# Performance work log

Measured on AMD Instinct MI355X. Metric: run time of the kernel, lower is better.

## Reference

```python
import jax, jax.numpy as jnp
import numpy as np

D_MODEL = 1024
NUM_HEADS = 16
KEY_SIZE = D_MODEL // NUM_HEADS
NEG_BIG = -1.0e9


def setup_inputs() -> dict:
    key = jax.random.key(0)
    ks = jax.random.split(key, 11)
    B, S = 2, 2048
    scale = 1.0 / np.sqrt(D_MODEL)
    inp = {
        "q": jax.random.normal(ks[0], (B, S, D_MODEL), dtype=jnp.float32),
        "v": jax.random.normal(ks[1], (B, S, D_MODEL), dtype=jnp.float32),
        "mask": jnp.ones((B, 1, S, S), dtype=jnp.float32),
        "wq_w": jax.random.normal(ks[2], (D_MODEL, D_MODEL), dtype=jnp.float32) * scale,
        "wq_b": jnp.zeros((D_MODEL,), dtype=jnp.float32),
        "wk_w": jax.random.normal(ks[3], (D_MODEL, D_MODEL), dtype=jnp.float32) * scale,
        "wk_b": jnp.zeros((D_MODEL,), dtype=jnp.float32),
        "wv_w": jax.random.normal(ks[4], (D_MODEL, D_MODEL), dtype=jnp.float32) * scale,
        "wv_b": jnp.zeros((D_MODEL,), dtype=jnp.float32),
        "wo_w": jax.random.normal(ks[5], (D_MODEL, D_MODEL), dtype=jnp.float32) * scale,
        "wo_b": jnp.zeros((D_MODEL,), dtype=jnp.float32),
    }
    return inp


def _split_heads(x, B):
    # [B, S, D] -> [B, H, S, K]
    S = x.shape[1]
    return x.reshape(B, S, NUM_HEADS, KEY_SIZE).transpose(0, 2, 1, 3)


def reference(q, v, mask, wq_w, wq_b, wk_w, wk_b, wv_w, wv_b, wo_w, wo_b):
    B = q.shape[0]
    query = _split_heads(q @ wq_w + wq_b, B)   # [B,H,Sq,K]
    key = _split_heads(v @ wk_w + wk_b, B)     # [B,H,Skv,K]
    value = _split_heads(v @ wv_w + wv_b, B)   # [B,H,Skv,K]

    score = jnp.einsum("bhqd,bhkd->bhqk", query, key) / jnp.sqrt(
        jnp.asarray(KEY_SIZE, dtype=jnp.float32)
    )
    # Original masking: multiply by mask, then replace exact zeros with -1e9.
    score = score * mask
    score = jnp.where(score == 0.0, jnp.float32(NEG_BIG), score)

    alignment = jax.nn.softmax(score, axis=-1)           # [B,H,Sq,Skv]
    context = jnp.einsum("bhqk,bhkd->bhqd", alignment, value)  # [B,H,Sq,K]
    context = context.transpose(0, 2, 1, 3).reshape(B, -1, D_MODEL)
    heads = context @ wo_w + wo_b
    return heads, alignment
```

## Files before the change

kernel.cpp:

```cpp
#include <hip/hip_runtime.h>
#include <cstddef>

#define D 1024
#define H 16
#define S 2048
#define B 2
#define M_ROWS (B * S)
#define NT 16
#define NEG_BIG_F (-1.0e9f)

typedef short bfrag __attribute__((ext_vector_type(8)));
typedef float f32x4 __attribute__((ext_vector_type(4)));

__device__ __forceinline__ unsigned short bf_rn(float x) {
    unsigned u = __float_as_uint(x);
    u += 0x7FFFu + ((u >> 16) & 1u);
    return (unsigned short)(u >> 16);
}
__device__ __forceinline__ float bf2f(unsigned short h) {
    return __uint_as_float(((unsigned)h) << 16);
}

__device__ __forceinline__ void load16(const float4* __restrict__ g, float (&x)[16]) {
#pragma unroll
    for (int q = 0; q < 4; q++) {
        float4 t = g[q];
        x[q*4+0] = t.x; x[q*4+1] = t.y; x[q*4+2] = t.z; x[q*4+3] = t.w;
    }
}

__device__ __forceinline__ void split16_store(const float (&x)[16],
                                              short* __restrict__ hp,
                                              short* __restrict__ lp) {
    __align__(16) short hs[16], ls[16];
#pragma unroll
    for (int e = 0; e < 16; e++) {
        unsigned short hh = bf_rn(x[e]);
        hs[e] = (short)hh;
        ls[e] = (short)bf_rn(x[e] - bf2f(hh));
    }
    *(bfrag*)(hp)     = *(const bfrag*)&hs[0];
    *(bfrag*)(hp + 8) = *(const bfrag*)&hs[8];
    *(bfrag*)(lp)     = *(const bfrag*)&ls[0];
    *(bfrag*)(lp + 8) = *(const bfrag*)&ls[8];
}

#define MFMA3(accv, AH, AL, BH, BL)                                          \
    accv = __builtin_amdgcn_mfma_f32_16x16x32_bf16(AH, BH, accv, 0, 0, 0);   \
    accv = __builtin_amdgcn_mfma_f32_16x16x32_bf16(AH, BL, accv, 0, 0, 0);   \
    accv = __builtin_amdgcn_mfma_f32_16x16x32_bf16(AL, BH, accv, 0, 0, 0);

__global__ __launch_bounds__(256) void transpose_w(
    const float* __restrict__ Win, float* __restrict__ WT)
{
    __shared__ float t[64][65];
    const int tid = threadIdx.x;
    const int bx = blockIdx.x * 64, by = blockIdx.y * 64;
    const int c = tid & 63, r0 = tid >> 6;
#pragma unroll
    for (int r = r0; r < 64; r += 4)
        t[r][c] = Win[(size_t)(by + r) * D + bx + c];
    __syncthreads();
#pragma unroll
    for (int r = r0; r < 64; r += 4)
        WT[(size_t)(bx + r) * D + by + c] = t[c][r];
}

#define PADK 72

__global__ __launch_bounds__(256) void mm_proj(
    const float* __restrict__ A, const float* __restrict__ WT,
    const float* __restrict__ bias, float* __restrict__ Cout, int mode)
{
    __shared__ __align__(16) short Ah[128][PADK], Al[128][PADK];
    __shared__ __align__(16) short Bh[64][PADK],  Bl[64][PADK];

    const int tid  = threadIdx.x;
    const int lane = tid & 63, wid = tid >> 6;
    const int wm = (wid >> 1) * 64, wn = (wid & 1) * 32;
    const int lr = lane >> 4, lc = lane & 15;
    const int tile_n = blockIdx.x * 64;
    const int tile_m = blockIdx.y * 128;

    f32x4 acc[4][2] = {};

    for (int k0 = 0; k0 < D; k0 += 64) {
        __syncthreads();
#pragma unroll
        for (int p = 0; p < 2; p++) {
            int s = tid + p * 256;
            int row = s >> 2, kseg = (s & 3) * 16;
            float x[16];
            load16((const float4*)&A[(size_t)(tile_m + row) * D + k0 + kseg], x);
            split16_store(x, &Ah[row][kseg], &Al[row][kseg]);
        }
        {
            int row = tid >> 2, kseg = (tid & 3) * 16;
            float x[16];
            load16((const float4*)&WT[(size_t)(tile_n + row) * D + k0 + kseg], x);
            split16_store(x, &Bh[row][kseg], &Bl[row][kseg]);
        }
        __syncthreads();
#pragma unroll
        for (int ks = 0; ks < 2; ks++) {
            const int ko = ks * 32 + lr * 8;
            bfrag ah[4], al[4], bh[2], bl[2];
#pragma unroll
            for (int fm = 0; fm < 4; fm++) {
                ah[fm] = *(const bfrag*)&Ah[wm + fm * 16 + lc][ko];
                al[fm] = *(const bfrag*)&Al[wm + fm * 16 + lc][ko];
            }
#pragma unroll
            for (int fn = 0; fn < 2; fn++) {
                bh[fn] = *(const bfrag*)&Bh[wn + fn * 16 + lc][ko];
                bl[fn] = *(const bfrag*)&Bl[wn + fn * 16 + lc][ko];
            }
#pragma unroll
            for (int fm = 0; fm < 4; fm++)
#pragma unroll
                for (int fn = 0; fn < 2; fn++) {
                    MFMA3(acc[fm][fn], ah[fm], al[fm], bh[fn], bl[fn])
                }
        }
    }

#pragma unroll
    for (int fm = 0; fm < 4; fm++)
#pragma unroll
        for (int fn = 0; fn < 2; fn++) {
            const int gm0 = tile_m + wm + fm * 16 + lr * 4;
            const int gn  = tile_n + wn + fn * 16 + lc;
            const float bv = bias[gn];
            if (mode == 2) {
                int bb = gm0 >> 11, ss = gm0 & (S - 1);
                int hh = gn >> 6,  dd = gn & 63;
                float4 o = {acc[fm][fn][0] + bv, acc[fm][fn][1] + bv,
                            acc[fm][fn][2] + bv, acc[fm][fn][3] + bv};
                *(float4*)&Cout[((size_t)(bb * H + hh) * 64 + dd) * S + ss] = o;
            } else {
#pragma unroll
                for (int r = 0; r < 4; r++) {
                    int gm = gm0 + r;
                    float val = acc[fm][fn][r] + bv;
                    if (mode == 0) {
                        Cout[(size_t)gm * D + gn] = val;
                    } else {
                        int bb = gm >> 11, ss = gm & (S - 1);
                        int hh = gn >> 6,  dd = gn & 63;
                        Cout[(((size_t)(bb * H + hh) * S + ss) << 6) + dd] = val;
                    }
                }
            }
        }
}

#define PADK32 40

__global__ __launch_bounds__(256) void scores_mm(
    const float* __restrict__ Q, const float* __restrict__ Kp,
    const float* __restrict__ mask, float* __restrict__ Sc,
    float2* __restrict__ aux)
{
    __shared__ __align__(16) short Qh[128][PADK32], Ql[128][PADK32];
    __shared__ __align__(16) short Kh[128][PADK32], Kl[128][PADK32];
    __shared__ float smx[2][128], sls[2][128];

    const int tid  = threadIdx.x;
    const int lane = tid & 63, wid = tid >> 6;
    const int wm = (wid >> 1) * 64, wn = (wid & 1) * 64;
    const int lr = lane >> 4, lc = lane & 15;
    const int bh = blockIdx.z, b = bh >> 4;
    const int tile_m = blockIdx.y * 128, tile_n = blockIdx.x * 128;

    const float* Qg = Q  + (((size_t)bh * S) << 6);
    const float* Kg = Kp + (((size_t)bh * S) << 6);

    f32x4 acc[4][4] = {};

    for (int k0 = 0; k0 < 64; k0 += 32) {
        __syncthreads();
        const int row = tid >> 1, kseg = (tid & 1) * 16;
        {
            float x[16];
            load16((const float4*)&Qg[((size_t)(tile_m + row) << 6) + k0 + kseg], x);
            split16_store(x, &Qh[row][kseg], &Ql[row][kseg]);
        }
        {
            float x[16];
            load16((const float4*)&Kg[((size_t)(tile_n + row) << 6) + k0 + kseg], x);
            split16_store(x, &Kh[row][kseg], &Kl[row][kseg]);
        }
        __syncthreads();
        const int ko = lr * 8;
        bfrag qh[4], ql[4], kh[4], kl[4];
#pragma unroll
        for (int fm = 0; fm < 4; fm++) {
            qh[fm] = *(const bfrag*)&Qh[wm + fm * 16 + lc][ko];
            ql[fm] = *(const bfrag*)&Ql[wm + fm * 16 + lc][ko];
        }
#pragma unroll
        for (int fn = 0; fn < 4; fn++) {
            kh[fn] = *(const bfrag*)&Kh[wn + fn * 16 + lc][ko];
            kl[fn] = *(const bfrag*)&Kl[wn + fn * 16 + lc][ko];
        }
#pragma unroll
        for (int fm = 0; fm < 4; fm++)
#pragma unroll
            for (int fn = 0; fn < 4; fn++) {
                MFMA3(acc[fm][fn], qh[fm], ql[fm], kh[fn], kl[fn])
            }
    }

    const float* mb = mask + (size_t)b * S * S;
    float* Sh = Sc + (size_t)bh * S * S;
#pragma unroll
    for (int fm = 0; fm < 4; fm++)
#pragma unroll
        for (int r = 0; r < 4; r++) {
            const int lrow = wm + fm * 16 + lr * 4 + r;
            const int gm = tile_m + lrow;
            float sc[4];
#pragma unroll
            for (int fn = 0; fn < 4; fn++) {
                const int gn = tile_n + wn + fn * 16 + lc;
                float v = acc[fm][fn][r] * 0.125f;
                v *= mb[(size_t)gm * S + gn];
                if (v == 0.0f) v = NEG_BIG_F;
                sc[fn] = v;
                Sh[(size_t)gm * S + gn] = v;
            }
            float mx = fmaxf(fmaxf(sc[0], sc[1]), fmaxf(sc[2], sc[3]));
#pragma unroll
            for (int d2 = 1; d2 < 16; d2 <<= 1) mx = fmaxf(mx, __shfl_xor(mx, d2));
            float ls = __expf(sc[0] - mx) + __expf(sc[1] - mx) +
                       __expf(sc[2] - mx) + __expf(sc[3] - mx);
#pragma unroll
            for (int d2 = 1; d2 < 16; d2 <<= 1) ls += __shfl_xor(ls, d2);
            if (lc == 0) { smx[wn >> 6][lrow] = mx; sls[wn >> 6][lrow] = ls; }
        }
    __syncthreads();
    if (tid < 128) {
        float m0 = smx[0][tid], m1 = smx[1][tid];
        float mx = fmaxf(m0, m1);
        float ls = sls[0][tid] * __expf(m0 - mx) + sls[1][tid] * __expf(m1 - mx);
        aux[((size_t)bh * S + tile_m + tid) * NT + blockIdx.x] = make_float2(mx, ls);
    }
}

__global__ __launch_bounds__(256) void reduce_stats(
    const float2* __restrict__ aux, float2* __restrict__ stats)
{
    const int row = blockIdx.x * 256 + threadIdx.x;
    const float2* a = aux + (size_t)row * NT;
    float m = -3.0e38f;
#pragma unroll
    for (int t = 0; t < NT; t++) m = fmaxf(m, a[t].x);
    float l = 0.0f;
#pragma unroll
    for (int t = 0; t < NT; t++) l += a[t].y * __expf(a[t].x - m);
    stats[row] = make_float2(m, 1.0f / l);
}

__global__ __launch_bounds__(256) void pv_mm(
    float* __restrict__ P, const float* __restrict__ VT,
    const float2* __restrict__ stats, float* __restrict__ Ctx)
{
    __shared__ __align__(16) short Ph[64][PADK], Pl[64][PADK];
    __shared__ __align__(16) short Vh[64][PADK], Vl[64][PADK];
    __shared__ float2 st[64];

    const int tid  = threadIdx.x;
    const int lane = tid & 63, wid = tid >> 6;
    const int wm = (wid >> 1) * 32, wn = (wid & 1) * 32;
    const int lr = lane >> 4, lc = lane & 15;
    const int tile_m = blockIdx.x * 64;
    const int bh = blockIdx.y, b = bh >> 4, h = bh & 15;

    float* Pg = P + (size_t)bh * S * S;
    const float* Vg = VT + (((size_t)bh) << 6) * S;

    if (tid < 64) st[tid] = stats[(size_t)bh * S + tile_m + tid];
    __syncthreads();

    const int prow = tid >> 2, pseg = (tid & 3) * 16;
    const float2 ms = st[prow];

    f32x4 acc[2][2] = {};

    for (int k0 = 0; k0 < S; k0 += 64) {
        {
            float4* gp = (float4*)&Pg[(size_t)(tile_m + prow) * S + k0 + pseg];
            float x[16];
#pragma unroll
            for (int q = 0; q < 4; q++) {
                float4 t = gp[q];
                t.x = __expf(t.x - ms.x) * ms.y;
                t.y = __expf(t.y - ms.x) * ms.y;
                t.z = __expf(t.z - ms.x) * ms.y;
                t.w = __expf(t.w - ms.x) * ms.y;
                gp[q] = t;
                x[q*4+0] = t.x; x[q*4+1] = t.y; x[q*4+2] = t.z; x[q*4+3] = t.w;
            }
            split16_store(x, &Ph[prow][pseg], &Pl[prow][pseg]);
        }
        {
            float x[16];
            load16((const float4*)&Vg[(size_t)prow * S + k0 + pseg], x);
            split16_store(x, &Vh[prow][pseg], &Vl[prow][pseg]);
        }
        __syncthreads();
#pragma unroll
        for (int ks = 0; ks < 2; ks++) {
            const int ko = ks * 32 + lr * 8;
            bfrag ah[2], al[2], bh2[2], bl2[2];
#pragma unroll
            for (int fm = 0; fm < 2; fm++) {
                ah[fm] = *(const bfrag*)&Ph[wm + fm * 16 + lc][ko];
                al[fm] = *(const bfrag*)&Pl[wm + fm * 16 + lc][ko];
            }
#pragma unroll
            for (int fn = 0; fn < 2; fn++) {
                bh2[fn] = *(const bfrag*)&Vh[wn + fn * 16 + lc][ko];
                bl2[fn] = *(const bfrag*)&Vl[wn + fn * 16 + lc][ko];
            }
#pragma unroll
            for (int fm = 0; fm < 2; fm++)
#pragma unroll
                for (int fn = 0; fn < 2; fn++) {
                    MFMA3(acc[fm][fn], ah[fm], al[fm], bh2[fn], bl2[fn])
                }
        }
        __syncthreads();
    }

#pragma unroll
    for (int fm = 0; fm < 2; fm++)
#pragma unroll
        for (int fn = 0; fn < 2; fn++)
#pragma unroll
            for (int r = 0; r < 4; r++) {
                int s_ = tile_m + wm + fm * 16 + lr * 4 + r;
                int dcol = h * 64 + wn + fn * 16 + lc;
                Ctx[((size_t)b * S + s_) * D + dcol] = acc[fm][fn][r];
            }
}

extern "C" void kernel_launch(void* const* d_in, const int* in_sizes, int n_in,
                              void* d_out, int out_size, void* d_ws, size_t ws_size,
                              hipStream_t stream)
{
    const float* q    = (const float*)d_in[0];
    const float* v    = (const float*)d_in[1];
    const float* mask = (const float*)d_in[2];
    const float* wq_w = (const float*)d_in[3];
    const float* wq_b = (const float*)d_in[4];
    const float* wk_w = (const float*)d_in[5];
    const float* wk_b = (const float*)d_in[6];
    const float* wv_w = (const float*)d_in[7];
    const float* wv_b = (const float*)d_in[8];
    const float* wo_w = (const float*)d_in[9];
    const float* wo_b = (const float*)d_in[10];

    float* out_heads = (float*)d_out;
    float* out_align = (float*)d_out + (size_t)B * S * D;

    float* wsf = (float*)d_ws;
    const size_t M1 = 1u << 20;
    float*  WT0 = wsf;
    float*  WT1 = wsf + M1;
    float*  WT2 = wsf + 2 * M1;
    float*  WT3 = wsf + 3 * M1;
    float*  Qw  = wsf + 4 * M1;
    float*  Kw  = wsf + 8 * M1;
    float*  VT  = wsf + 12 * M1;
    float*  Ctx = Qw;
    float2* aux   = (float2*)wsf;
    float2* stats = (float2*)(wsf + 2 * M1);

    dim3 tg(16, 16);
    transpose_w<<<tg, 256, 0, stream>>>(wq_w, WT0);
    transpose_w<<<tg, 256, 0, stream>>>(wk_w, WT1);
    transpose_w<<<tg, 256, 0, stream>>>(wv_w, WT2);
    transpose_w<<<tg, 256, 0, stream>>>(wo_w, WT3);

    dim3 pg(D / 64, M_ROWS / 128);
    mm_proj<<<pg, 256, 0, stream>>>(q, WT0, wq_b, Qw, 1);
    mm_proj<<<pg, 256, 0, stream>>>(v, WT1, wk_b, Kw, 1);
    mm_proj<<<pg, 256, 0, stream>>>(v, WT2, wv_b, VT, 2);

    dim3 sg(S / 128, S / 128, B * H);
    scores_mm<<<sg, 256, 0, stream>>>(Qw, Kw, mask, out_align, aux);

    reduce_stats<<<dim3((B * H * S) / 256), 256, 0, stream>>>(aux, stats);

    dim3 vg(S / 64, B * H);
    pv_mm<<<vg, 256, 0, stream>>>(out_align, VT, stats, Ctx);

    mm_proj<<<pg, 256, 0, stream>>>(Ctx, WT3, wo_b, out_heads, 0);
}
```

Baseline: 1.242 ms.

## Store pre-split bf16 hi/lo intermediates instead of fp32 between kernels

Weights, the Q/K/V projections and the context are now stored as pre-split bf16 high/low pairs in global memory. Consumer kernels can then copy tiles straight into shared memory without reloading fp32 and re-splitting them in every tile. The scores kernel loads the full 64-wide K dimension in one pass with a single barrier. The aux and stats buffers move into the output-heads region to free workspace, and the V-transpose epilogue loses its vectorized float4 store in favour of scalar short stores.

```diff
diff --git a/kernel.cpp b/kernel.cpp
--- a/kernel.cpp
+++ b/kernel.cpp
@@ -8,6 +8,7 @@
 #define M_ROWS (B * S)
 #define NT 16
 #define NEG_BIG_F (-1.0e9f)
+#define PADK 72
 
 typedef short bfrag __attribute__((ext_vector_type(8)));
 typedef float f32x4 __attribute__((ext_vector_type(4)));
@@ -45,13 +46,20 @@
     *(bfrag*)(lp + 8) = *(const bfrag*)&ls[8];
 }
 
+__device__ __forceinline__ void copy16(const unsigned short* __restrict__ g,
+                                       short* __restrict__ l) {
+    *(bfrag*)l       = *(const bfrag*)g;
+    *(bfrag*)(l + 8) = *(const bfrag*)(g + 8);
+}
+
 #define MFMA3(accv, AH, AL, BH, BL)                                          \
     accv = __builtin_amdgcn_mfma_f32_16x16x32_bf16(AH, BH, accv, 0, 0, 0);   \
     accv = __builtin_amdgcn_mfma_f32_16x16x32_bf16(AH, BL, accv, 0, 0, 0);   \
     accv = __builtin_amdgcn_mfma_f32_16x16x32_bf16(AL, BH, accv, 0, 0, 0);
 
-__global__ __launch_bounds__(256) void transpose_w(
-    const float* __restrict__ Win, float* __restrict__ WT)
+__global__ __launch_bounds__(256) void transpose_split_w(
+    const float* __restrict__ Win, unsigned short* __restrict__ WTh,
+    unsigned short* __restrict__ WTl)
 {
     __shared__ float t[64][65];
     const int tid = threadIdx.x;
@@ -62,15 +70,21 @@
         t[r][c] = Win[(size_t)(by + r) * D + bx + c];
     __syncthreads();
 #pragma unroll
-    for (int r = r0; r < 64; r += 4)
-        WT[(size_t)(bx + r) * D + by + c] = t[c][r];
-}
-
-#define PADK 72
+    for (int r = r0; r < 64; r += 4) {
+        float x = t[c][r];
+        unsigned short hh = bf_rn(x);
+        unsigned short ll = bf_rn(x - bf2f(hh));
+        WTh[(size_t)(bx + r) * D + by + c] = hh;
+        WTl[(size_t)(bx + r) * D + by + c] = ll;
+    }
+}
 
 __global__ __launch_bounds__(256) void mm_proj(
-    const float* __restrict__ A, const float* __restrict__ WT,
-    const float* __restrict__ bias, float* __restrict__ Cout, int mode)
+    const float* __restrict__ Af,
+    const unsigned short* __restrict__ Ah_g, const unsigned short* __restrict__ Al_g,
+    const unsigned short* __restrict__ WTh, const unsigned short* __restrict__ WTl,
+    const float* __restrict__ bias, float* __restrict__ Cf,
+    unsigned short* __restrict__ Ch, unsigned short* __restrict__ Cl, int mode)
 {
     __shared__ __align__(16) short Ah[128][PADK], Al[128][PADK];
     __shared__ __align__(16) short Bh[64][PADK],  Bl[64][PADK];
@@ -86,19 +100,28 @@
 
     for (int k0 = 0; k0 < D; k0 += 64) {
         __syncthreads();
-#pragma unroll
-        for (int p = 0; p < 2; p++) {
-            int s = tid + p * 256;
-            int row = s >> 2, kseg = (s & 3) * 16;
-            float x[16];
-            load16((const float4*)&A[(size_t)(tile_m + row) * D + k0 + kseg], x);
-            split16_store(x, &Ah[row][kseg], &Al[row][kseg]);
+        if (Af) {
+#pragma unroll
+            for (int p = 0; p < 2; p++) {
+                int s = tid + p * 256;
+                int row = s >> 2, kseg = (s & 3) * 16;
+                float x[16];
+                load16((const float4*)&Af[(size_t)(tile_m + row) * D + k0 + kseg], x);
+                split16_store(x, &Ah[row][kseg], &Al[row][kseg]);
+            }
+        } else {
+            int row = tid >> 1, off = (tid & 1) * 32;
+            const size_t ga = (size_t)(tile_m + row) * D + k0;
+            copy16(&Ah_g[ga + off],      &Ah[row][off]);
+            copy16(&Ah_g[ga + off + 16], &Ah[row][off + 16]);
+            copy16(&Al_g[ga + off],      &Al[row][off]);
+            copy16(&Al_g[ga + off + 16], &Al[row][off + 16]);
         }
         {
-            int row = tid >> 2, kseg = (tid & 3) * 16;
-            float x[16];
-            load16((const float4*)&WT[(size_t)(tile_n + row) * D + k0 + kseg], x);
-            split16_store(x, &Bh[row][kseg], &Bl[row][kseg]);
+            int row = tid >> 2, seg = (tid & 3) * 16;
+            const size_t gw = (size_t)(tile_n + row) * D + k0 + seg;
+            copy16(&WTh[gw], &Bh[row][seg]);
+            copy16(&WTl[gw], &Bl[row][seg]);
         }
         __syncthreads();
 #pragma unroll
@@ -131,38 +154,34 @@
             const int gm0 = tile_m + wm + fm * 16 + lr * 4;
             const int gn  = tile_n + wn + fn * 16 + lc;
             const float bv = bias[gn];
-            if (mode == 2) {
-                int bb = gm0 >> 11, ss = gm0 & (S - 1);
-                int hh = gn >> 6,  dd = gn & 63;
-                float4 o = {acc[fm][fn][0] + bv, acc[fm][fn][1] + bv,
-                            acc[fm][fn][2] + bv, acc[fm][fn][3] + bv};
-                *(float4*)&Cout[((size_t)(bb * H + hh) * 64 + dd) * S + ss] = o;
-            } else {
-#pragma unroll
-                for (int r = 0; r < 4; r++) {
-                    int gm = gm0 + r;
-                    float val = acc[fm][fn][r] + bv;
-                    if (mode == 0) {
-                        Cout[(size_t)gm * D + gn] = val;
-                    } else {
-                        int bb = gm >> 11, ss = gm & (S - 1);
-                        int hh = gn >> 6,  dd = gn & 63;
-                        Cout[(((size_t)(bb * H + hh) * S + ss) << 6) + dd] = val;
-                    }
+#pragma unroll
+            for (int r = 0; r < 4; r++) {
+                int gm = gm0 + r;
+                float val = acc[fm][fn][r] + bv;
+                if (mode == 0) {
+                    Cf[(size_t)gm * D + gn] = val;
+                } else {
+                    unsigned short hh = bf_rn(val);
+                    unsigned short ll = bf_rn(val - bf2f(hh));
+                    int bb = gm >> 11, ss = gm & (S - 1);
+                    int hd = gn >> 6,  dd = gn & 63;
+                    size_t a = (mode == 1)
+                        ? ((((size_t)(bb * H + hd) * S + ss) << 6) + dd)
+                        : ((((size_t)(bb * H + hd) << 6) + dd) * S + ss);
+                    Ch[a] = hh; Cl[a] = ll;
                 }
             }
         }
 }
 
-#define PADK32 40
-
 __global__ __launch_bounds__(256) void scores_mm(
-    const float* __restrict__ Q, const float* __restrict__ Kp,
+    const unsigned short* __restrict__ Qh_g, const unsigned short* __restrict__ Ql_g,
+    const unsigned short* __restrict__ Kh_g, const unsigned short* __restrict__ Kl_g,
     const float* __restrict__ mask, float* __restrict__ Sc,
     float2* __restrict__ aux)
 {
-    __shared__ __align__(16) short Qh[128][PADK32], Ql[128][PADK32];
-    __shared__ __align__(16) short Kh[128][PADK32], Kl[128][PADK32];
+    __shared__ __align__(16) short Qh[128][PADK], Ql[128][PADK];
+    __shared__ __align__(16) short Kh[128][PADK], Kl[128][PADK];
     __shared__ float smx[2][128], sls[2][128];
 
     const int tid  = threadIdx.x;
@@ -172,26 +191,25 @@
     const int bh = blockIdx.z, b = bh >> 4;
     const int tile_m = blockIdx.y * 128, tile_n = blockIdx.x * 128;
 
-    const float* Qg = Q  + (((size_t)bh * S) << 6);
-    const float* Kg = Kp + (((size_t)bh * S) << 6);
+    {
+        const int row = tid >> 1, off = (tid & 1) * 32;
+        const size_t gq = (((size_t)bh * S + tile_m + row) << 6);
+        const size_t gk = (((size_t)bh * S + tile_n + row) << 6);
+        copy16(&Qh_g[gq + off],      &Qh[row][off]);
+        copy16(&Qh_g[gq + off + 16], &Qh[row][off + 16]);
+        copy16(&Ql_g[gq + off],      &Ql[row][off]);
+        copy16(&Ql_g[gq + off + 16], &Ql[row][off + 16]);
+        copy16(&Kh_g[gk + off],      &Kh[row][off]);
+        copy16(&Kh_g[gk + off + 16], &Kh[row][off + 16]);
+        copy16(&Kl_g[gk + off],      &Kl[row][off]);
+        copy16(&Kl_g[gk + off + 16], &Kl[row][off + 16]);
+    }
+    __syncthreads();
 
     f32x4 acc[4][4] = {};
-
-    for (int k0 = 0; k0 < 64; k0 += 32) {
-        __syncthreads();
-        const int row = tid >> 1, kseg = (tid & 1) * 16;
-        {
-            float x[16];
-            load16((const float4*)&Qg[((size_t)(tile_m + row) << 6) + k0 + kseg], x);
-            split16_store(x, &Qh[row][kseg], &Ql[row][kseg]);
-        }
-        {
-            float x[16];
-            load16((const float4*)&Kg[((size_t)(tile_n + row) << 6) + k0 + kseg], x);
-            split16_store(x, &Kh[row][kseg], &Kl[row][kseg]);
-        }
-        __syncthreads();
-        const int ko = lr * 8;
+#pragma unroll
+    for (int ks = 0; ks < 2; ks++) {
+        const int ko = ks * 32 + lr * 8;
         bfrag qh[4], ql[4], kh[4], kl[4];
 #pragma unroll
         for (int fm = 0; fm < 4; fm++) {
@@ -262,8 +280,10 @@
 }
 
 __global__ __launch_bounds__(256) void pv_mm(
-    float* __restrict__ P, const float* __restrict__ VT,
-    const float2* __restrict__ stats, float* __restrict__ Ctx)
+    float* __restrict__ P,
+    const unsigned short* __restrict__ VTh_g, const unsigned short* __restrict__ VTl_g,
+    const float2* __restrict__ stats,
+    unsigned short* __restrict__ Ctxh, unsigned short* __restrict__ Ctxl)
 {
     __shared__ __align__(16) short Ph[64][PADK], Pl[64][PADK];
     __shared__ __align__(16) short Vh[64][PADK], Vl[64][PADK];
@@ -277,7 +297,7 @@
     const int bh = blockIdx.y, b = bh >> 4, h = bh & 15;
 
     float* Pg = P + (size_t)bh * S * S;
-    const float* Vg = VT + (((size_t)bh) << 6) * S;
+    const size_t vbase = ((size_t)bh << 6) * S;
 
     if (tid < 64) st[tid] = stats[(size_t)bh * S + tile_m + tid];
     __syncthreads();
@@ -304,9 +324,9 @@
             split16_store(x, &Ph[prow][pseg], &Pl[prow][pseg]);
         }
         {
-            float x[16];
-            load16((const float4*)&Vg[(size_t)prow * S + k0 + pseg], x);
-            split16_store(x, &Vh[prow][pseg], &Vl[prow][pseg]);
+            const size_t gv = vbase + (size_t)prow * S + k0 + pseg;
+            copy16(&VTh_g[gv], &Vh[prow][pseg]);
+            copy16(&VTl_g[gv], &Vl[prow][pseg]);
         }
         __syncthreads();
 #pragma unroll
@@ -340,8 +360,12 @@
 #pragma unroll
             for (int r = 0; r < 4; r++) {
                 int s_ = tile_m + wm + fm * 16 + lr * 4 + r;
-                int dcol = h * 64 + wn + fn * 16 + lc;
-                Ctx[((size_t)b * S + s_) * D + dcol] = acc[fm][fn][r];
+                int dcol = (h << 6) + wn + fn * 16 + lc;
+                float val = acc[fm][fn][r];
+                unsigned short hh = bf_rn(val);
+                unsigned short ll = bf_rn(val - bf2f(hh));
+                size_t a = ((size_t)b * S + s_) * D + dcol;
+                Ctxh[a] = hh; Ctxl[a] = ll;
             }
 }
 
@@ -364,37 +388,51 @@
     float* out_heads = (float*)d_out;
     float* out_align = (float*)d_out + (size_t)B * S * D;
 
-    float* wsf = (float*)d_ws;
-    const size_t M1 = 1u << 20;
-    float*  WT0 = wsf;
-    float*  WT1 = wsf + M1;
-    float*  WT2 = wsf + 2 * M1;
-    float*  WT3 = wsf + 3 * M1;
-    float*  Qw  = wsf + 4 * M1;
-    float*  Kw  = wsf + 8 * M1;
-    float*  VT  = wsf + 12 * M1;
-    float*  Ctx = Qw;
-    float2* aux   = (float2*)wsf;
-    float2* stats = (float2*)(wsf + 2 * M1);
+    const size_t qkv = (size_t)B * H * S * 64;
+    const size_t wsz = (size_t)D * D;
+    unsigned short* wsu = (unsigned short*)d_ws;
+    unsigned short* Qh  = wsu;
+    unsigned short* Ql  = Qh + qkv;
+    unsigned short* Kh  = Ql + qkv;
+    unsigned short* Kl  = Kh + qkv;
+    unsigned short* VTh = Kl + qkv;
+    unsigned short* VTl = VTh + qkv;
+    unsigned short* Wq_h = VTl + qkv;
+    unsigned short* Wq_l = Wq_h + wsz;
+    unsigned short* Wk_h = Wq_l + wsz;
+    unsigned short* Wk_l = Wk_h + wsz;
+    unsigned short* Wv_h = Wk_l + wsz;
+    unsigned short* Wv_l = Wv_h + wsz;
+    unsigned short* Wo_h = Wv_l + wsz;
+    unsigned short* Wo_l = Wo_h + wsz;
+    unsigned short* Ctxh = Qh;
+    unsigned short* Ctxl = Ql;
+
+    float2* aux   = (float2*)out_heads;
+    float2* stats = (float2*)(out_heads + (size_t)2 * 1024 * 1024 + 131072);
 
     dim3 tg(16, 16);
-    transpose_w<<<tg, 256, 0, stream>>>(wq_w, WT0);
-    transpose_w<<<tg, 256, 0, stream>>>(wk_w, WT1);
-    transpose_w<<<tg, 256, 0, stream>>>(wv_w, WT2);
-    transpose_w<<<tg, 256, 0, stream>>>(wo_w, WT3);
+    transpose_split_w<<<tg, 256, 0, stream>>>(wq_w, Wq_h, Wq_l);
+    transpose_split_w<<<tg, 256, 0, stream>>>(wk_w, Wk_h, Wk_l);
+    transpose_split_w<<<tg, 256, 0, stream>>>(wv_w, Wv_h, Wv_l);
+    transpose_split_w<<<tg, 256, 0, stream>>>(wo_w, Wo_h, Wo_l);
 
     dim3 pg(D / 64, M_ROWS / 128);
-    mm_proj<<<pg, 256, 0, stream>>>(q, WT0, wq_b, Qw, 1);
-    mm_proj<<<pg, 256, 0, stream>>>(v, WT1, wk_b, Kw, 1);
-    mm_proj<<<pg, 256, 0, stream>>>(v, WT2, wv_b, VT, 2);
+    mm_proj<<<pg, 256, 0, stream>>>(q, nullptr, nullptr, Wq_h, Wq_l, wq_b,
+                                    nullptr, Qh, Ql, 1);
+    mm_proj<<<pg, 256, 0, stream>>>(v, nullptr, nullptr, Wk_h, Wk_l, wk_b,
+                                    nullptr, Kh, Kl, 1);
+    mm_proj<<<pg, 256, 0, stream>>>(v, nullptr, nullptr, Wv_h, Wv_l, wv_b,
+                                    nullptr, VTh, VTl, 2);
 
     dim3 sg(S / 128, S / 128, B * H);
-    scores_mm<<<sg, 256, 0, stream>>>(Qw, Kw, mask, out_align, aux);
+    scores_mm<<<sg, 256, 0, stream>>>(Qh, Ql, Kh, Kl, mask, out_align, aux);
 
     reduce_stats<<<dim3((B * H * S) / 256), 256, 0, stream>>>(aux, stats);
 
     dim3 vg(S / 64, B * H);
-    pv_mm<<<vg, 256, 0, stream>>>(out_align, VT, stats, Ctx);
-
-    mm_proj<<<pg, 256, 0, stream>>>(Ctx, WT3, wo_b, out_heads, 0);
-}
+    pv_mm<<<vg, 256, 0, stream>>>(out_align, VTh, VTl, stats, Ctxh, Ctxl);
+
+    mm_proj<<<pg, 256, 0, stream>>>(nullptr, Ctxh, Ctxl, Wo_h, Wo_l, wo_b,
+                                    out_heads, nullptr, nullptr, 0);
+}
```

Measured after the change: 1.273 ms. 2.5% more time.
